# Optimization experiments

Hardware: AMD Instinct MI355X
Metric: run time of the kernel (lower is better)

Reference implementation:

```python
import jax, jax.numpy as jnp
import numpy as np

B, N, D = 8, 1024, 512
H = 8
DH = D // H
EPS_DIST = 1e-8
EPS_LN = 1e-5


def _layer_norm(x, gamma, beta):
    mu = jnp.mean(x, axis=-1, keepdims=True)
    var = jnp.mean((x - mu) ** 2, axis=-1, keepdims=True)
    return (x - mu) * jax.lax.rsqrt(var + EPS_LN) * gamma + beta


def setup_inputs() -> dict:
    key = jax.random.key(0)
    ks = jax.random.split(key, 6)
    scale = 1.0 / np.sqrt(D)
    inp = {
        "x": jax.random.normal(ks[0], (B, N, D), dtype=jnp.float32),
        "Wq": jax.random.normal(ks[1], (D, D), dtype=jnp.float32) * scale,
        "Wk": jax.random.normal(ks[2], (D, D), dtype=jnp.float32) * scale,
        "Wv": jax.random.normal(ks[3], (D, D), dtype=jnp.float32) * scale,
        "Wo": jax.random.normal(ks[4], (D, D), dtype=jnp.float32) * scale,
        "bq": jnp.zeros((D,), jnp.float32),
        "bk": jnp.zeros((D,), jnp.float32),
        "bv": jnp.zeros((D,), jnp.float32),
        "bo": jnp.zeros((D,), jnp.float32),
        "ln1_g": jnp.ones((D,), jnp.float32),
        "ln1_b": jnp.zeros((D,), jnp.float32),
        "ln2_g": jnp.ones((D,), jnp.float32),
        "ln2_b": jnp.zeros((D,), jnp.float32),
    }
    return inp


def reference(x, Wq, bq, Wk, bk, Wv, bv, Wo, bo, ln1_g, ln1_b, ln2_g, ln2_b):
    residual = x
    h = _layer_norm(x, ln1_g, ln1_b)  # pre-norm

    def heads(t):
        # [B,N,D] -> [B,H,N,DH]
        return t.reshape(B, N, H, DH).transpose(0, 2, 1, 3)

    q = heads(h @ Wq + bq)
    k = heads(h @ Wk + bk)
    v = heads(h @ Wv + bv)

    # Euclidean pairwise distance via ||q||^2 + ||k||^2 - 2 q.k expansion
    q_sq = jnp.sum(q * q, axis=-1)[..., :, None]      # [B,H,N,1]
    k_sq = jnp.sum(k * k, axis=-1)[..., None, :]      # [B,H,1,N]
    qk = jnp.einsum("bhnd,bhmd->bhnm", q, k)          # [B,H,N,N]
    d2 = jnp.maximum(q_sq + k_sq - 2.0 * qk, 0.0)
    dist = jnp.sqrt(d2 + EPS_DIST)

    # distance -> attention score: smaller distance = higher attention
    attn = jax.nn.softmax(-dist, axis=-1)             # [B,H,N,N]

    out = jnp.einsum("bhnm,bhmd->bhnd", attn, v)      # [B,H,N,DH]
    out = out.transpose(0, 2, 1, 3).reshape(B, N, D)
    out = out @ Wo + bo

    y = residual + out
    y = _layer_norm(y, ln2_g, ln2_b)
    return y
```

## Files before the change

### kernel.cpp

```cpp
#include <hip/hip_runtime.h>
#include <math.h>

typedef __attribute__((ext_vector_type(8))) short short8;
typedef __attribute__((ext_vector_type(4))) float f32x4;

constexpr int B  = 8;
constexpr int N  = 1024;
constexpr int D  = 512;
constexpr int H  = 8;
constexpr int DH = 64;
constexpr int M_ROWS = 8192;
constexpr float EPS_DIST = 1e-8f;
constexpr float EPS_LN   = 1e-5f;

__device__ inline unsigned short bfbits(float f) {
    union { float f; unsigned u; } v; v.f = f;
    unsigned r = v.u + 0x7fffu + ((v.u >> 16) & 1u);
    return (unsigned short)(r >> 16);
}
__device__ inline float bf2f(unsigned short s) {
    union { unsigned u; float f; } v; v.u = ((unsigned)s) << 16; return v.f;
}

__device__ inline void async_ld16(unsigned short* lds, const unsigned short* g) {
    __builtin_amdgcn_global_load_lds(
        (const __attribute__((address_space(1))) unsigned int*)(g),
        (__attribute__((address_space(3))) unsigned int*)(lds),
        16, 0, 0);
}

__global__ __launch_bounds__(256) void wconv_kernel(const float* __restrict__ Wq,
                                                    const float* __restrict__ Wk,
                                                    const float* __restrict__ Wv,
                                                    const float* __restrict__ Wo,
                                                    unsigned short* __restrict__ WtAll) {
    int bx = blockIdx.x;
    int sub = bx >> 6;
    const float* W = sub == 0 ? Wq : sub == 1 ? Wk : sub == 2 ? Wv : Wo;
    unsigned short* Wt = WtAll + (size_t)sub * 262144;
    int t = (bx & 63) * 256 + threadIdx.x;
    int tn = t & 127, tk = t >> 7;
    int k = tk * 4, n = tn * 4;
    float4 r0 = *(const float4*)&W[(size_t)(k + 0) * 512 + n];
    float4 r1 = *(const float4*)&W[(size_t)(k + 1) * 512 + n];
    float4 r2 = *(const float4*)&W[(size_t)(k + 2) * 512 + n];
    float4 r3 = *(const float4*)&W[(size_t)(k + 3) * 512 + n];
    ushort4 c;
    c.x = bfbits(r0.x); c.y = bfbits(r1.x); c.z = bfbits(r2.x); c.w = bfbits(r3.x);
    *(ushort4*)&Wt[(size_t)(n + 0) * 512 + k] = c;
    c.x = bfbits(r0.y); c.y = bfbits(r1.y); c.z = bfbits(r2.y); c.w = bfbits(r3.y);
    *(ushort4*)&Wt[(size_t)(n + 1) * 512 + k] = c;
    c.x = bfbits(r0.z); c.y = bfbits(r1.z); c.z = bfbits(r2.z); c.w = bfbits(r3.z);
    *(ushort4*)&Wt[(size_t)(n + 2) * 512 + k] = c;
    c.x = bfbits(r0.w); c.y = bfbits(r1.w); c.z = bfbits(r2.w); c.w = bfbits(r3.w);
    *(ushort4*)&Wt[(size_t)(n + 3) * 512 + k] = c;
}

__device__ inline float block_sum256(float s, float* red) {
    for (int o = 32; o > 0; o >>= 1) s += __shfl_down(s, o, 64);
    int lane = threadIdx.x & 63, wid = threadIdx.x >> 6;
    if (lane == 0) red[wid] = s;
    __syncthreads();
    if (threadIdx.x == 0) red[4] = red[0] + red[1] + red[2] + red[3];
    __syncthreads();
    return red[4];
}

template <int OUT_BF16, int IN_BF16>
__global__ __launch_bounds__(256) void ln_kernel(const void* __restrict__ xv,
                                                 const float* __restrict__ res,
                                                 const float* __restrict__ gamma,
                                                 const float* __restrict__ beta,
                                                 void* __restrict__ out) {
    __shared__ float red[8];
    const int row = blockIdx.x;
    const int t = threadIdx.x;
    float v0, v1;
    if (IN_BF16) {
        const unsigned short* xr = (const unsigned short*)xv + (size_t)row * D;
        v0 = bf2f(xr[t]); v1 = bf2f(xr[t + 256]);
    } else {
        const float* xr = (const float*)xv + (size_t)row * D;
        v0 = xr[t]; v1 = xr[t + 256];
    }
    if (res) {
        const float* rr = res + (size_t)row * D;
        v0 += rr[t]; v1 += rr[t + 256];
    }
    float mu = block_sum256(v0 + v1, red) * (1.0f / D);
    float d0 = v0 - mu, d1 = v1 - mu;
    float var = block_sum256(d0 * d0 + d1 * d1, red) * (1.0f / D);
    float rstd = rsqrtf(var + EPS_LN);
    float o0 = d0 * rstd * gamma[t] + beta[t];
    float o1 = d1 * rstd * gamma[t + 256] + beta[t + 256];
    if (OUT_BF16) {
        ((unsigned short*)out)[(size_t)row * D + t]       = bfbits(o0);
        ((unsigned short*)out)[(size_t)row * D + t + 256] = bfbits(o1);
    } else {
        ((float*)out)[(size_t)row * D + t]       = o0;
        ((float*)out)[(size_t)row * D + t + 256] = o1;
    }
}

template <int MODE, int MT>
__global__ __launch_bounds__(256) void gemm128(const unsigned short* __restrict__ A,
                                               const unsigned short* __restrict__ Wt,
                                               const float* __restrict__ bias0,
                                               const float* __restrict__ bias1,
                                               const float* __restrict__ bias2,
                                               void* __restrict__ o0,
                                               unsigned short* __restrict__ Ko,
                                               unsigned short* __restrict__ Vo,
                                               float* __restrict__ sq0,
                                               float* __restrict__ sq1) {
    constexpr int RB = M_ROWS / MT;
    constexpr int NI = MT / 32;
    constexpr int SMSZ = (MODE == 1) ? 18432 : (MT * 32 + 4096);
    __shared__ unsigned short smem[SMSZ];
    unsigned short* As = smem;
    unsigned short* Bs = smem + MT * 32;

    const int id = blockIdx.x;
    const int by = id & (RB - 1), bx = id / RB;
    const int tid = threadIdx.x;
    const int lane = tid & 63, wv = tid >> 6;
    const int quad = lane >> 4, l15 = lane & 15;
    const int row0 = by * MT, col0 = bx * 128;
    const int wm = (wv & 1) * (MT / 2), wn = (wv >> 1) * 64;

    f32x4 acc[NI][4];
    #pragma unroll
    for (int i = 0; i < NI; ++i)
        #pragma unroll
        for (int j = 0; j < 4; ++j) acc[i][j] = (f32x4){0.f, 0.f, 0.f, 0.f};

    const unsigned short* Ag = A  + (size_t)row0 * 512;
    const unsigned short* Bg = Wt + (size_t)col0 * 512;

    for (int k0 = 0; k0 < 512; k0 += 32) {
        __syncthreads();
        #pragma unroll
        for (int c = 0; c < MT * 32 / 2048; ++c) {
            int fu = c * 2048 + tid * 8;
            int r = fu >> 5, ko = fu & 31;
            async_ld16(As + fu, Ag + (size_t)r * 512 + k0 + ko);
        }
        #pragma unroll
        for (int c = 0; c < 2; ++c) {
            int fu = c * 2048 + tid * 8;
            int r = fu >> 5, ko = fu & 31;
            async_ld16(Bs + fu, Bg + (size_t)r * 512 + k0 + ko);
        }
        __syncthreads();

        short8 af[NI], bf[4];
        #pragma unroll
        for (int i = 0; i < NI; ++i)
            af[i] = *(const short8*)&As[(wm + i * 16 + l15) * 32 + quad * 8];
        #pragma unroll
        for (int j = 0; j < 4; ++j)
            bf[j] = *(const short8*)&Bs[(wn + j * 16 + l15) * 32 + quad * 8];
        #pragma unroll
        for (int i = 0; i < NI; ++i)
            #pragma unroll
            for (int j = 0; j < 4; ++j)
                acc[i][j] = __builtin_amdgcn_mfma_f32_16x16x32_bf16(af[i], bf[j], acc[i][j], 0, 0, 0);
    }

    if (MODE == 0) {
        unsigned short* C = (unsigned short*)o0;
        #pragma unroll
        for (int i = 0; i < NI; ++i)
            #pragma unroll
            for (int j = 0; j < 4; ++j) {
                int col = col0 + wn + j * 16 + l15;
                float bv = bias0[col];
                #pragma unroll
                for (int r = 0; r < 4; ++r) {
                    int row = row0 + wm + i * 16 + quad * 4 + r;
                    C[(size_t)row * 512 + col] = bfbits(acc[i][j][r] + bv);
                }
            }
    } else {
        const int colg = col0 + wn;
        const int seg = colg >> 9;
        const int hh = (colg & 511) >> 6;
        const float* bias = seg == 0 ? bias0 : seg == 1 ? bias1 : bias2;

        if (seg < 2) {
            unsigned short* dst = seg == 0 ? (unsigned short*)o0 : Ko;
            float* sq = seg == 0 ? sq0 : sq1;
            #pragma unroll
            for (int i = 0; i < NI; ++i) {
                const int m0 = row0 + wm + i * 16 + quad * 4;
                float ss[4] = {0.f, 0.f, 0.f, 0.f};
                #pragma unroll
                for (int j = 0; j < 4; ++j) {
                    float bvj = bias[hh * 64 + j * 16 + l15];
                    #pragma unroll
                    for (int r = 0; r < 4; ++r) {
                        float v = acc[i][j][r] + bvj;
                        unsigned short ub = bfbits(v);
                        float vr = bf2f(ub);
                        ss[r] += vr * vr;
                        int m = m0 + r;
                        int b_ = m >> 10, n_ = m & 1023;
                        dst[((size_t)((b_ * 8 + hh) * 1024) + n_) * 64 + j * 16 + l15] = ub;
                    }
                }
                #pragma unroll
                for (int r = 0; r < 4; ++r) {
                    float s = ss[r];
                    s += __shfl_xor(s, 1, 64);
                    s += __shfl_xor(s, 2, 64);
                    s += __shfl_xor(s, 4, 64);
                    s += __shfl_xor(s, 8, 64);
                    if (l15 == 0) {
                        int m = m0 + r;
                        sq[(size_t)((m >> 10) * 8 + hh) * 1024 + (m & 1023)] = s;
                    }
                }
            }
        } else {
            __syncthreads();
            unsigned short* T = smem + wv * 4608;
            #pragma unroll
            for (int i = 0; i < NI; ++i)
                #pragma unroll
                for (int j = 0; j < 4; ++j) {
                    float bvj = bias[hh * 64 + j * 16 + l15];
                    ushort4 pk;
                    pk.x = bfbits(acc[i][j][0] + bvj);
                    pk.y = bfbits(acc[i][j][1] + bvj);
                    pk.z = bfbits(acc[i][j][2] + bvj);
                    pk.w = bfbits(acc[i][j][3] + bvj);
                    *(ushort4*)&T[(j * 16 + l15) * 72 + i * 16 + quad * 4] = pk;
                }
            const int b_ = (row0 + wm) >> 10;
            const int nbase = (row0 + wm) & 1023;
            unsigned short* Vg = Vo + ((size_t)((b_ * 8 + hh) * 64)) * 1024 + nbase;
            #pragma unroll
            for (int it = 0; it < 8; ++it) {
                int dl = it * 8 + (lane >> 3);
                int nl = (lane & 7) * 8;
                uint4 v = *(const uint4*)&T[dl * 72 + nl];
                *(uint4*)&Vg[(size_t)dl * 1024 + nl] = v;
            }
        }
    }
}

__global__ __launch_bounds__(256) void attn_kernel(const unsigned short* __restrict__ Q,
                                                   const unsigned short* __restrict__ K,
                                                   const unsigned short* __restrict__ Vt,
                                                   const float* __restrict__ qsq,
                                                   const float* __restrict__ ksq,
                                                   unsigned short* __restrict__ O) {
    __shared__ unsigned short Ks[2][64][72];
    __shared__ unsigned short Vs[2][64][72];
    __shared__ unsigned short Ps[4][32][72];
    __shared__ float ksq_s[2][64];

    const int id = blockIdx.x;
    const int bh = id & 63, qb = id >> 6;
    const int q0 = qb * 128;
    const int tid = threadIdx.x;
    const int lane = tid & 63, w = tid >> 6;
    const int quad = lane >> 4, l15 = lane & 15;
    const int b_ = bh >> 3, h_ = bh & 7;

    const unsigned short* Qb = Q  + (size_t)bh * N * DH;
    const unsigned short* Kb = K  + (size_t)bh * N * DH;
    const unsigned short* Vb = Vt + (size_t)bh * DH * N;

    short8 qf[2][2];
    #pragma unroll
    for (int i = 0; i < 2; ++i) {
        const unsigned short* qp = Qb + (size_t)(q0 + w * 32 + i * 16 + l15) * 64 + quad * 8;
        qf[i][0] = *(const short8*)qp;
        qf[i][1] = *(const short8*)(qp + 32);
    }
    float qe[2][4];
    #pragma unroll
    for (int i = 0; i < 2; ++i)
        #pragma unroll
        for (int r = 0; r < 4; ++r)
            qe[i][r] = qsq[bh * N + q0 + w * 32 + i * 16 + quad * 4 + r] + EPS_DIST;

    f32x4 oacc[2][4];
    #pragma unroll
    for (int i = 0; i < 2; ++i)
        #pragma unroll
        for (int dt = 0; dt < 4; ++dt) oacc[i][dt] = (f32x4){0.f, 0.f, 0.f, 0.f};
    float dpart[2][4] = {};

    const int rr = tid >> 2, cc = (tid & 3) * 16;
    uint4 kreg0, kreg1, vreg0, vreg1;
    float ksreg = 0.f;

    {
        const unsigned short* kg = Kb + (size_t)rr * 64 + cc;
        kreg0 = *(const uint4*)kg; kreg1 = *(const uint4*)(kg + 8);
        const unsigned short* vg = Vb + (size_t)rr * N + cc;
        vreg0 = *(const uint4*)vg; vreg1 = *(const uint4*)(vg + 8);
        if (tid < 64) ksreg = ksq[bh * N + tid];
    }
    *(uint4*)&Ks[0][rr][cc]     = kreg0;
    *(uint4*)&Ks[0][rr][cc + 8] = kreg1;
    *(uint4*)&Vs[0][rr][cc]     = vreg0;
    *(uint4*)&Vs[0][rr][cc + 8] = vreg1;
    if (tid < 64) ksq_s[0][tid] = ksreg;
    __syncthreads();

    for (int kt = 0; kt < 16; ++kt) {
        const int cur = kt & 1;
        if (kt < 15) {
            const unsigned short* kg = Kb + (size_t)((kt + 1) * 64 + rr) * 64 + cc;
            kreg0 = *(const uint4*)kg; kreg1 = *(const uint4*)(kg + 8);
            const unsigned short* vg = Vb + (size_t)rr * N + (kt + 1) * 64 + cc;
            vreg0 = *(const uint4*)vg; vreg1 = *(const uint4*)(vg + 8);
            if (tid < 64) ksreg = ksq[bh * N + (kt + 1) * 64 + tid];
        }

        #pragma unroll
        for (int kb = 0; kb < 4; ++kb) {
            short8 kf0 = *(const short8*)&Ks[cur][kb * 16 + l15][quad * 8];
            short8 kf1 = *(const short8*)&Ks[cur][kb * 16 + l15][32 + quad * 8];
            float ks2 = ksq_s[cur][kb * 16 + l15];
            #pragma unroll
            for (int i = 0; i < 2; ++i) {
                f32x4 sa = (f32x4){0.f, 0.f, 0.f, 0.f};
                sa = __builtin_amdgcn_mfma_f32_16x16x32_bf16(qf[i][0], kf0, sa, 0, 0, 0);
                sa = __builtin_amdgcn_mfma_f32_16x16x32_bf16(qf[i][1], kf1, sa, 0, 0, 0);
                #pragma unroll
                for (int r = 0; r < 4; ++r) {
                    float d2 = fmaf(-2.0f, sa[r], qe[i][r] + ks2);
                    d2 = fmaxf(d2, EPS_DIST);
                    float p = __expf(-__builtin_amdgcn_sqrtf(d2));
                    dpart[i][r] += p;
                    Ps[w][i * 16 + quad * 4 + r][kb * 16 + l15] = bfbits(p);
                }
            }
        }

        short8 vf[4][2];
        #pragma unroll
        for (int dt = 0; dt < 4; ++dt)
            #pragma unroll
            for (int kc = 0; kc < 2; ++kc)
                vf[dt][kc] = *(const short8*)&Vs[cur][dt * 16 + l15][kc * 32 + quad * 8];
        #pragma unroll
        for (int i = 0; i < 2; ++i)
            #pragma unroll
            for (int kc = 0; kc < 2; ++kc) {
                short8 pf = *(const short8*)&Ps[w][i * 16 + l15][kc * 32 + quad * 8];
                #pragma unroll
                for (int dt = 0; dt < 4; ++dt)
                    oacc[i][dt] = __builtin_amdgcn_mfma_f32_16x16x32_bf16(pf, vf[dt][kc], oacc[i][dt], 0, 0, 0);
            }

        if (kt < 15) {
            *(uint4*)&Ks[cur ^ 1][rr][cc]     = kreg0;
            *(uint4*)&Ks[cur ^ 1][rr][cc + 8] = kreg1;
            *(uint4*)&Vs[cur ^ 1][rr][cc]     = vreg0;
            *(uint4*)&Vs[cur ^ 1][rr][cc + 8] = vreg1;
            if (tid < 64) ksq_s[cur ^ 1][tid] = ksreg;
        }
        __syncthreads();
    }

    float rinv[2][4];
    #pragma unroll
    for (int i = 0; i < 2; ++i)
        #pragma unroll
        for (int r = 0; r < 4; ++r) {
            float s = dpart[i][r];
            s += __shfl_xor(s, 1, 64);
            s += __shfl_xor(s, 2, 64);
            s += __shfl_xor(s, 4, 64);
            s += __shfl_xor(s, 8, 64);
            rinv[i][r] = 1.0f / s;
        }

    #pragma unroll
    for (int i = 0; i < 2; ++i)
        #pragma unroll
        for (int dt = 0; dt < 4; ++dt)
            #pragma unroll
            for (int r = 0; r < 4; ++r) {
                int n_ = q0 + w * 32 + i * 16 + quad * 4 + r;
                O[((size_t)(b_ * N + n_) * D) + h_ * DH + dt * 16 + l15] =
                    bfbits(oacc[i][dt][r] * rinv[i][r]);
            }
}

extern "C" void kernel_launch(void* const* d_in, const int* in_sizes, int n_in,
                              void* d_out, int out_size, void* d_ws, size_t ws_size,
                              hipStream_t stream) {
    const float* x     = (const float*)d_in[0];
    const float* Wq    = (const float*)d_in[1];
    const float* Wk    = (const float*)d_in[2];
    const float* Wv    = (const float*)d_in[3];
    const float* Wo    = (const float*)d_in[4];
    const float* bq    = (const float*)d_in[5];
    const float* bk    = (const float*)d_in[6];
    const float* bv    = (const float*)d_in[7];
    const float* bo    = (const float*)d_in[8];
    const float* ln1_g = (const float*)d_in[9];
    const float* ln1_b = (const float*)d_in[10];
    const float* ln2_g = (const float*)d_in[11];
    const float* ln2_b = (const float*)d_in[12];
    float* out = (float*)d_out;

    unsigned short* WtAll = (unsigned short*)d_ws;
    unsigned short* h_bf  = WtAll + 4 * 262144;
    unsigned short* Qb    = h_bf + 4194304;
    unsigned short* Kb    = Qb + 4194304;
    unsigned short* Vtg   = Kb + 4194304;
    unsigned short* Ob    = Vtg + 4194304;
    unsigned short* Y0    = Ob + 4194304;
    float* qsq = (float*)(Y0 + 4194304);
    float* ksq = qsq + 65536;

    wconv_kernel<<<256, 256, 0, stream>>>(Wq, Wk, Wv, Wo, WtAll);

    ln_kernel<1, 0><<<M_ROWS, 256, 0, stream>>>(x, nullptr, ln1_g, ln1_b, h_bf);

    gemm128<1, 128><<<768, 256, 0, stream>>>(h_bf, WtAll, bq, bk, bv,
                                             Qb, Kb, Vtg, qsq, ksq);

    attn_kernel<<<512, 256, 0, stream>>>(Qb, Kb, Vtg, qsq, ksq, Ob);

    gemm128<0, 64><<<512, 256, 0, stream>>>(Ob, WtAll + 3 * 262144, bo,
                                            nullptr, nullptr, Y0,
                                            nullptr, nullptr, nullptr, nullptr);

    ln_kernel<0, 1><<<M_ROWS, 256, 0, stream>>>(Y0, x, ln2_g, ln2_b, out);
}
```

Baseline: 188.7 us.

## Merge prep kernels, deepen GEMM K-step, widen attention block to 512 threads

Merges the weight transpose/convert kernel and the first LayerNorm into one launch, and splits the second LayerNorm into its own specialized kernel. The GEMM now loads 64-wide K tiles, halving the number of loop iterations and barriers per tile. Attention blocks grow to 8 waves of 16 query rows each, so each thread loads one 16-byte K/V chunk and holds fewer accumulators. P is now converted to bf16 by truncation instead of rounding, which is cheaper but slightly less accurate. GEMM LDS use grows, and the larger attention blocks change occupancy.

```diff
diff --git a/kernel.cpp b/kernel.cpp
--- a/kernel.cpp
+++ b/kernel.cpp
@@ -29,33 +29,6 @@
         16, 0, 0);
 }
 
-__global__ __launch_bounds__(256) void wconv_kernel(const float* __restrict__ Wq,
-                                                    const float* __restrict__ Wk,
-                                                    const float* __restrict__ Wv,
-                                                    const float* __restrict__ Wo,
-                                                    unsigned short* __restrict__ WtAll) {
-    int bx = blockIdx.x;
-    int sub = bx >> 6;
-    const float* W = sub == 0 ? Wq : sub == 1 ? Wk : sub == 2 ? Wv : Wo;
-    unsigned short* Wt = WtAll + (size_t)sub * 262144;
-    int t = (bx & 63) * 256 + threadIdx.x;
-    int tn = t & 127, tk = t >> 7;
-    int k = tk * 4, n = tn * 4;
-    float4 r0 = *(const float4*)&W[(size_t)(k + 0) * 512 + n];
-    float4 r1 = *(const float4*)&W[(size_t)(k + 1) * 512 + n];
-    float4 r2 = *(const float4*)&W[(size_t)(k + 2) * 512 + n];
-    float4 r3 = *(const float4*)&W[(size_t)(k + 3) * 512 + n];
-    ushort4 c;
-    c.x = bfbits(r0.x); c.y = bfbits(r1.x); c.z = bfbits(r2.x); c.w = bfbits(r3.x);
-    *(ushort4*)&Wt[(size_t)(n + 0) * 512 + k] = c;
-    c.x = bfbits(r0.y); c.y = bfbits(r1.y); c.z = bfbits(r2.y); c.w = bfbits(r3.y);
-    *(ushort4*)&Wt[(size_t)(n + 1) * 512 + k] = c;
-    c.x = bfbits(r0.z); c.y = bfbits(r1.z); c.z = bfbits(r2.z); c.w = bfbits(r3.z);
-    *(ushort4*)&Wt[(size_t)(n + 2) * 512 + k] = c;
-    c.x = bfbits(r0.w); c.y = bfbits(r1.w); c.z = bfbits(r2.w); c.w = bfbits(r3.w);
-    *(ushort4*)&Wt[(size_t)(n + 3) * 512 + k] = c;
-}
-
 __device__ inline float block_sum256(float s, float* red) {
     for (int o = 32; o > 0; o >>= 1) s += __shfl_down(s, o, 64);
     int lane = threadIdx.x & 63, wid = threadIdx.x >> 6;
@@ -66,40 +39,69 @@
     return red[4];
 }
 
-template <int OUT_BF16, int IN_BF16>
-__global__ __launch_bounds__(256) void ln_kernel(const void* __restrict__ xv,
-                                                 const float* __restrict__ res,
-                                                 const float* __restrict__ gamma,
-                                                 const float* __restrict__ beta,
-                                                 void* __restrict__ out) {
+__global__ __launch_bounds__(256) void prep_kernel(const float* __restrict__ Wq,
+                                                   const float* __restrict__ Wk,
+                                                   const float* __restrict__ Wv,
+                                                   const float* __restrict__ Wo,
+                                                   unsigned short* __restrict__ WtAll,
+                                                   const float* __restrict__ x,
+                                                   const float* __restrict__ ln1_g,
+                                                   const float* __restrict__ ln1_b,
+                                                   unsigned short* __restrict__ h_bf) {
+    __shared__ float red[8];
+    const int bxg = blockIdx.x;
+    if (bxg < 256) {
+        int sub = bxg >> 6;
+        const float* W = sub == 0 ? Wq : sub == 1 ? Wk : sub == 2 ? Wv : Wo;
+        unsigned short* Wt = WtAll + (size_t)sub * 262144;
+        int t = (bxg & 63) * 256 + threadIdx.x;
+        int tn = t & 127, tk = t >> 7;
+        int k = tk * 4, n = tn * 4;
+        float4 r0 = *(const float4*)&W[(size_t)(k + 0) * 512 + n];
+        float4 r1 = *(const float4*)&W[(size_t)(k + 1) * 512 + n];
+        float4 r2 = *(const float4*)&W[(size_t)(k + 2) * 512 + n];
+        float4 r3 = *(const float4*)&W[(size_t)(k + 3) * 512 + n];
+        ushort4 c;
+        c.x = bfbits(r0.x); c.y = bfbits(r1.x); c.z = bfbits(r2.x); c.w = bfbits(r3.x);
+        *(ushort4*)&Wt[(size_t)(n + 0) * 512 + k] = c;
+        c.x = bfbits(r0.y); c.y = bfbits(r1.y); c.z = bfbits(r2.y); c.w = bfbits(r3.y);
+        *(ushort4*)&Wt[(size_t)(n + 1) * 512 + k] = c;
+        c.x = bfbits(r0.z); c.y = bfbits(r1.z); c.z = bfbits(r2.z); c.w = bfbits(r3.z);
+        *(ushort4*)&Wt[(size_t)(n + 2) * 512 + k] = c;
+        c.x = bfbits(r0.w); c.y = bfbits(r1.w); c.z = bfbits(r2.w); c.w = bfbits(r3.w);
+        *(ushort4*)&Wt[(size_t)(n + 3) * 512 + k] = c;
+    } else {
+        const int row = bxg - 256;
+        const int t = threadIdx.x;
+        const float* xr = x + (size_t)row * D;
+        float v0 = xr[t], v1 = xr[t + 256];
+        float mu = block_sum256(v0 + v1, red) * (1.0f / D);
+        float d0 = v0 - mu, d1 = v1 - mu;
+        float var = block_sum256(d0 * d0 + d1 * d1, red) * (1.0f / D);
+        float rstd = rsqrtf(var + EPS_LN);
+        h_bf[(size_t)row * D + t]       = bfbits(d0 * rstd * ln1_g[t] + ln1_b[t]);
+        h_bf[(size_t)row * D + t + 256] = bfbits(d1 * rstd * ln1_g[t + 256] + ln1_b[t + 256]);
+    }
+}
+
+__global__ __launch_bounds__(256) void ln2_kernel(const unsigned short* __restrict__ y0,
+                                                  const float* __restrict__ res,
+                                                  const float* __restrict__ gamma,
+                                                  const float* __restrict__ beta,
+                                                  float* __restrict__ out) {
     __shared__ float red[8];
     const int row = blockIdx.x;
     const int t = threadIdx.x;
-    float v0, v1;
-    if (IN_BF16) {
-        const unsigned short* xr = (const unsigned short*)xv + (size_t)row * D;
-        v0 = bf2f(xr[t]); v1 = bf2f(xr[t + 256]);
-    } else {
-        const float* xr = (const float*)xv + (size_t)row * D;
-        v0 = xr[t]; v1 = xr[t + 256];
-    }
-    if (res) {
-        const float* rr = res + (size_t)row * D;
-        v0 += rr[t]; v1 += rr[t + 256];
-    }
+    const unsigned short* xr = y0 + (size_t)row * D;
+    const float* rr = res + (size_t)row * D;
+    float v0 = bf2f(xr[t]) + rr[t];
+    float v1 = bf2f(xr[t + 256]) + rr[t + 256];
     float mu = block_sum256(v0 + v1, red) * (1.0f / D);
     float d0 = v0 - mu, d1 = v1 - mu;
     float var = block_sum256(d0 * d0 + d1 * d1, red) * (1.0f / D);
     float rstd = rsqrtf(var + EPS_LN);
-    float o0 = d0 * rstd * gamma[t] + beta[t];
-    float o1 = d1 * rstd * gamma[t + 256] + beta[t + 256];
-    if (OUT_BF16) {
-        ((unsigned short*)out)[(size_t)row * D + t]       = bfbits(o0);
-        ((unsigned short*)out)[(size_t)row * D + t + 256] = bfbits(o1);
-    } else {
-        ((float*)out)[(size_t)row * D + t]       = o0;
-        ((float*)out)[(size_t)row * D + t + 256] = o1;
-    }
+    out[(size_t)row * D + t]       = d0 * rstd * gamma[t] + beta[t];
+    out[(size_t)row * D + t + 256] = d1 * rstd * gamma[t + 256] + beta[t + 256];
 }
 
 template <int MODE, int MT>
@@ -115,10 +117,12 @@
                                                float* __restrict__ sq1) {
     constexpr int RB = M_ROWS / MT;
     constexpr int NI = MT / 32;
-    constexpr int SMSZ = (MODE == 1) ? 18432 : (MT * 32 + 4096);
+    constexpr int ASZ = MT * 64, BSZ = 128 * 64;
+    constexpr int SMSZ = (MODE == 1) ? ((ASZ + BSZ > 18432) ? ASZ + BSZ : 18432)
+                                     : (ASZ + BSZ);
     __shared__ unsigned short smem[SMSZ];
     unsigned short* As = smem;
-    unsigned short* Bs = smem + MT * 32;
+    unsigned short* Bs = smem + ASZ;
 
     const int id = blockIdx.x;
     const int by = id & (RB - 1), bx = id / RB;
@@ -137,34 +141,37 @@
     const unsigned short* Ag = A  + (size_t)row0 * 512;
     const unsigned short* Bg = Wt + (size_t)col0 * 512;
 
-    for (int k0 = 0; k0 < 512; k0 += 32) {
+    for (int k0 = 0; k0 < 512; k0 += 64) {
         __syncthreads();
         #pragma unroll
-        for (int c = 0; c < MT * 32 / 2048; ++c) {
+        for (int c = 0; c < ASZ / 2048; ++c) {
             int fu = c * 2048 + tid * 8;
-            int r = fu >> 5, ko = fu & 31;
+            int r = fu >> 6, ko = fu & 63;
             async_ld16(As + fu, Ag + (size_t)r * 512 + k0 + ko);
         }
         #pragma unroll
-        for (int c = 0; c < 2; ++c) {
+        for (int c = 0; c < BSZ / 2048; ++c) {
             int fu = c * 2048 + tid * 8;
-            int r = fu >> 5, ko = fu & 31;
+            int r = fu >> 6, ko = fu & 63;
             async_ld16(Bs + fu, Bg + (size_t)r * 512 + k0 + ko);
         }
         __syncthreads();
 
-        short8 af[NI], bf[4];
-        #pragma unroll
-        for (int i = 0; i < NI; ++i)
-            af[i] = *(const short8*)&As[(wm + i * 16 + l15) * 32 + quad * 8];
-        #pragma unroll
-        for (int j = 0; j < 4; ++j)
-            bf[j] = *(const short8*)&Bs[(wn + j * 16 + l15) * 32 + quad * 8];
-        #pragma unroll
-        for (int i = 0; i < NI; ++i)
+        #pragma unroll
+        for (int ks = 0; ks < 2; ++ks) {
+            short8 af[NI], bf[4];
+            #pragma unroll
+            for (int i = 0; i < NI; ++i)
+                af[i] = *(const short8*)&As[(wm + i * 16 + l15) * 64 + ks * 32 + quad * 8];
             #pragma unroll
             for (int j = 0; j < 4; ++j)
-                acc[i][j] = __builtin_amdgcn_mfma_f32_16x16x32_bf16(af[i], bf[j], acc[i][j], 0, 0, 0);
+                bf[j] = *(const short8*)&Bs[(wn + j * 16 + l15) * 64 + ks * 32 + quad * 8];
+            #pragma unroll
+            for (int i = 0; i < NI; ++i)
+                #pragma unroll
+                for (int j = 0; j < 4; ++j)
+                    acc[i][j] = __builtin_amdgcn_mfma_f32_16x16x32_bf16(af[i], bf[j], acc[i][j], 0, 0, 0);
+        }
     }
 
     if (MODE == 0) {
@@ -250,7 +257,7 @@
     }
 }
 
-__global__ __launch_bounds__(256) void attn_kernel(const unsigned short* __restrict__ Q,
+__global__ __launch_bounds__(512) void attn_kernel(const unsigned short* __restrict__ Q,
                                                    const unsigned short* __restrict__ K,
                                                    const unsigned short* __restrict__ Vt,
                                                    const float* __restrict__ qsq,
@@ -258,7 +265,7 @@
                                                    unsigned short* __restrict__ O) {
     __shared__ unsigned short Ks[2][64][72];
     __shared__ unsigned short Vs[2][64][72];
-    __shared__ unsigned short Ps[4][32][72];
+    __shared__ unsigned short Ps[8][16][72];
     __shared__ float ksq_s[2][64];
 
     const int id = blockIdx.x;
@@ -273,52 +280,40 @@
     const unsigned short* Kb = K  + (size_t)bh * N * DH;
     const unsigned short* Vb = Vt + (size_t)bh * DH * N;
 
-    short8 qf[2][2];
+    short8 qf0, qf1;
+    {
+        const unsigned short* qp = Qb + (size_t)(q0 + w * 16 + l15) * 64 + quad * 8;
+        qf0 = *(const short8*)qp;
+        qf1 = *(const short8*)(qp + 32);
+    }
+    float qe[4];
     #pragma unroll
-    for (int i = 0; i < 2; ++i) {
-        const unsigned short* qp = Qb + (size_t)(q0 + w * 32 + i * 16 + l15) * 64 + quad * 8;
-        qf[i][0] = *(const short8*)qp;
-        qf[i][1] = *(const short8*)(qp + 32);
-    }
-    float qe[2][4];
+    for (int r = 0; r < 4; ++r)
+        qe[r] = qsq[bh * N + q0 + w * 16 + quad * 4 + r] + EPS_DIST;
+
+    f32x4 oacc[4];
     #pragma unroll
-    for (int i = 0; i < 2; ++i)
-        #pragma unroll
-        for (int r = 0; r < 4; ++r)
-            qe[i][r] = qsq[bh * N + q0 + w * 32 + i * 16 + quad * 4 + r] + EPS_DIST;
-
-    f32x4 oacc[2][4];
-    #pragma unroll
-    for (int i = 0; i < 2; ++i)
-        #pragma unroll
-        for (int dt = 0; dt < 4; ++dt) oacc[i][dt] = (f32x4){0.f, 0.f, 0.f, 0.f};
-    float dpart[2][4] = {};
-
-    const int rr = tid >> 2, cc = (tid & 3) * 16;
-    uint4 kreg0, kreg1, vreg0, vreg1;
+    for (int dt = 0; dt < 4; ++dt) oacc[dt] = (f32x4){0.f, 0.f, 0.f, 0.f};
+    float dpart[4] = {};
+
+    const int rr = tid >> 3, cc = (tid & 7) * 8;
+    uint4 kreg, vreg;
     float ksreg = 0.f;
 
-    {
-        const unsigned short* kg = Kb + (size_t)rr * 64 + cc;
-        kreg0 = *(const uint4*)kg; kreg1 = *(const uint4*)(kg + 8);
-        const unsigned short* vg = Vb + (size_t)rr * N + cc;
-        vreg0 = *(const uint4*)vg; vreg1 = *(const uint4*)(vg + 8);
-        if (tid < 64) ksreg = ksq[bh * N + tid];
-    }
-    *(uint4*)&Ks[0][rr][cc]     = kreg0;
-    *(uint4*)&Ks[0][rr][cc + 8] = kreg1;
-    *(uint4*)&Vs[0][rr][cc]     = vreg0;
-    *(uint4*)&Vs[0][rr][cc + 8] = vreg1;
+    kreg = *(const uint4*)(Kb + (size_t)rr * 64 + cc);
+    vreg = *(const uint4*)(Vb + (size_t)rr * N + cc);
+    if (tid < 64) ksreg = ksq[bh * N + tid];
+
+    *(uint4*)&Ks[0][rr][cc] = kreg;
+    *(uint4*)&Vs[0][rr][cc] = vreg;
     if (tid < 64) ksq_s[0][tid] = ksreg;
     __syncthreads();
 
     for (int kt = 0; kt < 16; ++kt) {
         const int cur = kt & 1;
         if (kt < 15) {
-            const unsigned short* kg = Kb + (size_t)((kt + 1) * 64 + rr) * 64 + cc;
-            kreg0 = *(const uint4*)kg; kreg1 = *(const uint4*)(kg + 8);
-            const unsigned short* vg = Vb + (size_t)rr * N + (kt + 1) * 64 + cc;
-            vreg0 = *(const uint4*)vg; vreg1 = *(const uint4*)(vg + 8);
+            kreg = *(const uint4*)(Kb + (size_t)((kt + 1) * 64 + rr) * 64 + cc);
+            vreg = *(const uint4*)(Vb + (size_t)rr * N + (kt + 1) * 64 + cc);
             if (tid < 64) ksreg = ksq[bh * N + (kt + 1) * 64 + tid];
         }
 
@@ -327,19 +322,17 @@
             short8 kf0 = *(const short8*)&Ks[cur][kb * 16 + l15][quad * 8];
             short8 kf1 = *(const short8*)&Ks[cur][kb * 16 + l15][32 + quad * 8];
             float ks2 = ksq_s[cur][kb * 16 + l15];
-            #pragma unroll
-            for (int i = 0; i < 2; ++i) {
-                f32x4 sa = (f32x4){0.f, 0.f, 0.f, 0.f};
-                sa = __builtin_amdgcn_mfma_f32_16x16x32_bf16(qf[i][0], kf0, sa, 0, 0, 0);
-                sa = __builtin_amdgcn_mfma_f32_16x16x32_bf16(qf[i][1], kf1, sa, 0, 0, 0);
-                #pragma unroll
-                for (int r = 0; r < 4; ++r) {
-                    float d2 = fmaf(-2.0f, sa[r], qe[i][r] + ks2);
-                    d2 = fmaxf(d2, EPS_DIST);
-                    float p = __expf(-__builtin_amdgcn_sqrtf(d2));
-                    dpart[i][r] += p;
-                    Ps[w][i * 16 + quad * 4 + r][kb * 16 + l15] = bfbits(p);
-                }
+            f32x4 sa = (f32x4){0.f, 0.f, 0.f, 0.f};
+            sa = __builtin_amdgcn_mfma_f32_16x16x32_bf16(qf0, kf0, sa, 0, 0, 0);
+            sa = __builtin_amdgcn_mfma_f32_16x16x32_bf16(qf1, kf1, sa, 0, 0, 0);
+            #pragma unroll
+            for (int r = 0; r < 4; ++r) {
+                float d2 = fmaf(-2.0f, sa[r], qe[r] + ks2);
+                d2 = fmaxf(d2, EPS_DIST);
+                float p = __expf(-__builtin_amdgcn_sqrtf(d2));
+                dpart[r] += p;
+                union { float f; unsigned u; } pu; pu.f = p;
+                Ps[w][quad * 4 + r][kb * 16 + l15] = (unsigned short)(pu.u >> 16);
             }
         }
 
@@ -350,48 +343,40 @@
             for (int kc = 0; kc < 2; ++kc)
                 vf[dt][kc] = *(const short8*)&Vs[cur][dt * 16 + l15][kc * 32 + quad * 8];
         #pragma unroll
-        for (int i = 0; i < 2; ++i)
-            #pragma unroll
-            for (int kc = 0; kc < 2; ++kc) {
-                short8 pf = *(const short8*)&Ps[w][i * 16 + l15][kc * 32 + quad * 8];
-                #pragma unroll
-                for (int dt = 0; dt < 4; ++dt)
-                    oacc[i][dt] = __builtin_amdgcn_mfma_f32_16x16x32_bf16(pf, vf[dt][kc], oacc[i][dt], 0, 0, 0);
-            }
+        for (int kc = 0; kc < 2; ++kc) {
+            short8 pf = *(const short8*)&Ps[w][l15][kc * 32 + quad * 8];
+            #pragma unroll
+            for (int dt = 0; dt < 4; ++dt)
+                oacc[dt] = __builtin_amdgcn_mfma_f32_16x16x32_bf16(pf, vf[dt][kc], oacc[dt], 0, 0, 0);
+        }
 
         if (kt < 15) {
-            *(uint4*)&Ks[cur ^ 1][rr][cc]     = kreg0;
-            *(uint4*)&Ks[cur ^ 1][rr][cc + 8] = kreg1;
-            *(uint4*)&Vs[cur ^ 1][rr][cc]     = vreg0;
-            *(uint4*)&Vs[cur ^ 1][rr][cc + 8] = vreg1;
+            *(uint4*)&Ks[cur ^ 1][rr][cc] = kreg;
+            *(uint4*)&Vs[cur ^ 1][rr][cc] = vreg;
             if (tid < 64) ksq_s[cur ^ 1][tid] = ksreg;
         }
         __syncthreads();
     }
 
-    float rinv[2][4];
+    float rinv[4];
     #pragma unroll
-    for (int i = 0; i < 2; ++i)
+    for (int r = 0; r < 4; ++r) {
+        float s = dpart[r];
+        s += __shfl_xor(s, 1, 64);
+        s += __shfl_xor(s, 2, 64);
+        s += __shfl_xor(s, 4, 64);
+        s += __shfl_xor(s, 8, 64);
+        rinv[r] = 1.0f / s;
+    }
+
+    #pragma unroll
+    for (int dt = 0; dt < 4; ++dt)
         #pragma unroll
         for (int r = 0; r < 4; ++r) {
-            float s = dpart[i][r];
-            s += __shfl_xor(s, 1, 64);
-            s += __shfl_xor(s, 2, 64);
-            s += __shfl_xor(s, 4, 64);
-            s += __shfl_xor(s, 8, 64);
-            rinv[i][r] = 1.0f / s;
-        }
-
-    #pragma unroll
-    for (int i = 0; i < 2; ++i)
-        #pragma unroll
-        for (int dt = 0; dt < 4; ++dt)
-            #pragma unroll
-            for (int r = 0; r < 4; ++r) {
-                int n_ = q0 + w * 32 + i * 16 + quad * 4 + r;
-                O[((size_t)(b_ * N + n_) * D) + h_ * DH + dt * 16 + l15] =
-                    bfbits(oacc[i][dt][r] * rinv[i][r]);
-            }
+            int n_ = q0 + w * 16 + quad * 4 + r;
+            O[((size_t)(b_ * N + n_) * D) + h_ * DH + dt * 16 + l15] =
+                bfbits(oacc[dt][r] * rinv[r]);
+        }
 }
 
 extern "C" void kernel_launch(void* const* d_in, const int* in_sizes, int n_in,
@@ -422,18 +407,17 @@
     float* qsq = (float*)(Y0 + 4194304);
     float* ksq = qsq + 65536;
 
-    wconv_kernel<<<256, 256, 0, stream>>>(Wq, Wk, Wv, Wo, WtAll);
-
-    ln_kernel<1, 0><<<M_ROWS, 256, 0, stream>>>(x, nullptr, ln1_g, ln1_b, h_bf);
+    prep_kernel<<<256 + M_ROWS, 256, 0, stream>>>(Wq, Wk, Wv, Wo, WtAll,
+                                                  x, ln1_g, ln1_b, h_bf);
 
     gemm128<1, 128><<<768, 256, 0, stream>>>(h_bf, WtAll, bq, bk, bv,
                                              Qb, Kb, Vtg, qsq, ksq);
 
-    attn_kernel<<<512, 256, 0, stream>>>(Qb, Kb, Vtg, qsq, ksq, Ob);
+    attn_kernel<<<512, 512, 0, stream>>>(Qb, Kb, Vtg, qsq, ksq, Ob);
 
     gemm128<0, 64><<<512, 256, 0, stream>>>(Ob, WtAll + 3 * 262144, bo,
                                             nullptr, nullptr, Y0,
                                             nullptr, nullptr, nullptr, nullptr);
 
-    ln_kernel<0, 1><<<M_ROWS, 256, 0, stream>>>(Y0, x, ln2_g, ln2_b, out);
-}
+    ln2_kernel<<<M_ROWS, 256, 0, stream>>>(Y0, x, ln2_g, ln2_b, out);
+}
```

Result: faster. 182.8 us (-3.1%).
